# Optimization experiments

Hardware: AMD Instinct MI355X
Metric: run time of the kernel (lower is better)

The kernel has to match this reference:

```python
import jax, jax.numpy as jnp
import numpy as np

B, S, D, DFF = 4, 2048, 1024, 4096
EPS = 1e-5


def layernorm(x, gamma, beta):
    mu = jnp.mean(x, axis=-1, keepdims=True)
    var = jnp.var(x, axis=-1, keepdims=True)
    return (x - mu) * jax.lax.rsqrt(var + EPS) * gamma + beta


def attention(Q, K, V, causal):
    d_k = Q.shape[-1]
    scores = jnp.einsum('bqd,bkd->bqk', Q, K) / jnp.sqrt(jnp.asarray(d_k, Q.dtype))
    if causal:
        q_len, k_len = scores.shape[-2], scores.shape[-1]
        mask = jnp.tril(jnp.ones((q_len, k_len), dtype=bool))
        scores = jnp.where(mask[None], scores, jnp.asarray(-jnp.inf, scores.dtype))
    w = jax.nn.softmax(scores, axis=-1)
    return jnp.einsum('bqk,bkd->bqd', w, V)


def setup_inputs() -> dict:
    key = jax.random.key(0)
    ks = jax.random.split(key, 12)
    sd = 0.02
    return {
        'y': jax.random.normal(ks[0], (B, S, D), jnp.float32),
        'Z': jax.random.normal(ks[1], (B, S, D), jnp.float32),
        'w1': jax.random.normal(ks[2], (D, DFF), jnp.float32) * sd,
        'b1': jnp.zeros((DFF,), jnp.float32),
        'w2': jax.random.normal(ks[3], (DFF, D), jnp.float32) * sd,
        'b2': jnp.zeros((D,), jnp.float32),
        'g1': jnp.ones((D,), jnp.float32), 'beta1': jnp.zeros((D,), jnp.float32),
        'g2': jnp.ones((D,), jnp.float32), 'beta2': jnp.zeros((D,), jnp.float32),
        'g3': jnp.ones((D,), jnp.float32), 'beta3': jnp.zeros((D,), jnp.float32),
    }


def reference(y, Z, w1, b1, w2, b2, g1, beta1, g2, beta2, g3, beta3):
    # masked (causal) self-attention, single head over full d_model
    sa = attention(y, y, y, causal=True)
    y = layernorm(y + sa, g1, beta1)
    # cross-attention to encoder memory Z
    ca = attention(y, Z, Z, causal=False)
    y = layernorm(y + ca, g2, beta2)
    # position-wise FFN
    h = jax.nn.relu(jnp.einsum('bsd,df->bsf', y, w1) + b1)
    ff = jnp.einsum('bsf,fd->bsd', h, w2) + b2
    y = layernorm(y + ff, g3, beta3)
    return y
```

## Files before the change

### kernel.cpp

```cpp
#include <hip/hip_runtime.h>
#include <hip/hip_bf16.h>


#define Bb 4
#define Ss 2048
#define Dd 1024
#define Ff 4096

typedef __attribute__((ext_vector_type(4))) float f32x4;
typedef __attribute__((ext_vector_type(8))) short bf16x8;
typedef __attribute__((ext_vector_type(8))) unsigned short u16x8;
typedef __attribute__((ext_vector_type(4))) unsigned short u16x4;

__device__ __forceinline__ unsigned short f2bf(float f) {
  unsigned u = __float_as_uint(f);
  u += 0x7FFFu + ((u >> 16) & 1u);
  return (unsigned short)(u >> 16);
}
__device__ __forceinline__ float bf2f(unsigned short h) {
  return __uint_as_float(((unsigned)h) << 16);
}

__device__ __forceinline__ void gload_lds16(const void* g, void* l) {
  __builtin_amdgcn_global_load_lds((const __attribute__((address_space(1))) void*)g,
                                   (__attribute__((address_space(3))) void*)l, 16, 0, 0);
}

__device__ __forceinline__ int xcd8(int orig, int n) {
  int q = n >> 3, r = n & 7;
  int x = orig & 7;
  int base = x < r ? x * (q + 1) : r * (q + 1) + (x - r) * q;
  return base + (orig >> 3);
}

__global__ __launch_bounds__(256) void k_transpose_cast(const float* __restrict__ in,
                                                        unsigned short* __restrict__ outT,
                                                        unsigned short* __restrict__ outR,
                                                        int R, int C) {
  __shared__ float t[32][33];
  size_t bo = (size_t)blockIdx.z * R * C;
  const float* pin = in + bo;
  unsigned short* poutT = outT + bo;
  unsigned short* poutR = outR ? outR + bo : nullptr;
  int c0 = blockIdx.x * 32, r0 = blockIdx.y * 32;
  int tx = threadIdx.x, ty = threadIdx.y;
#pragma unroll
  for (int i = 0; i < 4; i++) {
    float v = pin[(size_t)(r0 + ty + i * 8) * C + c0 + tx];
    t[ty + i * 8][tx] = v;
    if (poutR) poutR[(size_t)(r0 + ty + i * 8) * C + c0 + tx] = f2bf(v);
  }
  __syncthreads();
#pragma unroll
  for (int i = 0; i < 4; i++)
    poutT[(size_t)(c0 + ty + i * 8) * R + r0 + tx] = f2bf(t[tx][ty + i * 8]);
}

#define BAR() __builtin_amdgcn_s_barrier()
#define PRIO1() __builtin_amdgcn_s_setprio(1)
#define PRIO0() __builtin_amdgcn_s_setprio(0)
#define LGKM0()                                          \
  {                                                      \
    asm volatile("s_waitcnt lgkmcnt(0)" ::: "memory");   \
    __builtin_amdgcn_sched_barrier(0);                   \
  }

#define LDA8(arr, mh, bo)                                                       \
  {                                                                             \
    _Pragma("unroll") for (int j_ = 0; j_ < QM; ++j_) {                         \
      _Pragma("unroll") for (int kh_ = 0; kh_ < 2; ++kh_) {                     \
        arr[j_][kh_] =                                                          \
            *(const bf16x8*)(lds + (bo) + ((mh)*QM + j_) * 2048 + aof[kh_]);    \
      }                                                                         \
    }                                                                           \
  }

#define LDB8(arr, nh, bo)                                                       \
  {                                                                             \
    _Pragma("unroll") for (int n_ = 0; n_ < 2; ++n_) {                          \
      _Pragma("unroll") for (int kh_ = 0; kh_ < 2; ++kh_) {                     \
        arr[n_][kh_] =                                                          \
            *(const bf16x8*)(lds + (bo) + ((nh)*2 + n_) * 2048 + bof[kh_]);     \
      }                                                                         \
    }                                                                           \
  }

#define MMQ(aarr, barr, mh, nh)                                                 \
  {                                                                             \
    _Pragma("unroll") for (int j_ = 0; j_ < QM; ++j_) {                         \
      _Pragma("unroll") for (int n_ = 0; n_ < 2; ++n_) {                        \
        _Pragma("unroll") for (int kh_ = 0; kh_ < 2; ++kh_) {                   \
          acc[(mh)*QM + j_][(nh)*2 + n_] = __builtin_amdgcn_mfma_f32_16x16x32_bf16( \
              aarr[j_][kh_], barr[n_][kh_], acc[(mh)*QM + j_][(nh)*2 + n_], 0, 0, 0); \
        }                                                                       \
      }                                                                         \
    }                                                                           \
  }

#define EPILOGUE(MR_, WMS_)                                                     \
  {                                                                             \
    const int colb = j0 + wc * 64 + fr;                                         \
    const int rowb = i0 + wr * (WMS_) + (kq << 2);                              \
    const size_t cb = (size_t)bz * bsC;                                         \
    _Pragma("unroll") for (int m = 0; m < (MR_); ++m) {                         \
      _Pragma("unroll") for (int r = 0; r < 4; ++r) {                           \
        size_t ro = cb + (size_t)(rowb + m * 16 + r) * ldc;                     \
        _Pragma("unroll") for (int n = 0; n < 4; ++n) {                         \
          float v = acc[m][n][r];                                               \
          int col = colb + n * 16;                                              \
          if (EPI == 0) Cb[ro + col] = f2bf(v * scale);                         \
          else if (EPI == 1) Cf[ro + col] = v;                                  \
          else if (EPI == 2) Cb[ro + col] = f2bf(fmaxf(v + bias[col], 0.f));    \
          else Cf[ro + col] = v + bias[col];                                    \
        }                                                                       \
      }                                                                         \
    }                                                                           \
  }

template <int EPI, bool CAUSAL>
__global__ __launch_bounds__(512) void k_gemm8(
    const unsigned short* __restrict__ Ag, const unsigned short* __restrict__ Bg,
    float* __restrict__ Cf, unsigned short* __restrict__ Cb,
    const float* __restrict__ bias, int K, int lda, int ldb, int ldc,
    long bsA, long bsB, long bsC, float scale) {
  constexpr int QM = 4;
  constexpr int ABYTES = 32768, BBYTES = 32768;
  __shared__ alignas(16) char lds[2 * ABYTES + 2 * BBYTES];

  int i0, j0;
  if (CAUSAL) {
    int t = xcd8(blockIdx.x, gridDim.x);
    int ti = (int)((sqrtf(8.f * t + 1.f) - 1.f) * 0.5f);
    while ((ti + 1) * (ti + 2) / 2 <= t) ++ti;
    while (ti * (ti + 1) / 2 > t) --ti;
    i0 = ti * 256;
    j0 = (t - ti * (ti + 1) / 2) * 256;
  } else {
    int lin = xcd8(blockIdx.y * gridDim.x + blockIdx.x, gridDim.x * gridDim.y);
    i0 = (lin / gridDim.x) * 256;
    j0 = (lin % gridDim.x) * 256;
  }
  int bz = blockIdx.z;
  Ag += (size_t)bz * bsA;
  Bg += (size_t)bz * bsB;

  const int nk = K / 64;
  const int niter = nk / 2;

  const int tid = threadIdx.x;
  const int w = tid >> 6, lane = tid & 63;
  const int wr = w >> 2, wc = w & 3;

  const int srow = (w << 3) + (lane >> 3);
  const int bcs = (lane & 7) ^ (lane >> 3);
  const unsigned short* As = Ag + (size_t)(i0 + srow) * lda + bcs * 8;
  const unsigned short* Bs = Bg + (size_t)(j0 + srow) * ldb + bcs * 8;
  char* ldsAw = lds + w * 1024;
  char* ldsBw = lds + 2 * ABYTES + w * 1024;

  auto stA = [&](int kt, int hf) {
    int ks = kt < nk ? kt : nk - 1;
#pragma unroll
    for (int l = 0; l < 2; ++l)
      gload_lds16(As + (size_t)(hf * 128 + l * 64) * lda + ks * 64,
                  ldsAw + (kt & 1) * ABYTES + hf * 128 * 128 + l * 8192);
  };
  auto stB = [&](int kt, int hf) {
    int ks = kt < nk ? kt : nk - 1;
#pragma unroll
    for (int l = 0; l < 2; ++l)
      gload_lds16(Bs + (size_t)(hf * 128 + l * 64) * ldb + ks * 64,
                  ldsBw + (kt & 1) * BBYTES + hf * 128 * 128 + l * 8192);
  };

  const int fr = lane & 15, kq = lane >> 4;
  const int rA = wr * 128 + fr;
  const int rB = wc * 64 + fr;
  unsigned aof[2], bof[2];
  aof[0] = rA * 128 + ((kq ^ (rA & 7)) << 4);
  aof[1] = rA * 128 + (((kq + 4) ^ (rA & 7)) << 4);
  bof[0] = 2 * ABYTES + rB * 128 + ((kq ^ (rB & 7)) << 4);
  bof[1] = 2 * ABYTES + rB * 128 + (((kq + 4) ^ (rB & 7)) << 4);
  constexpr int A0 = 0, A1 = ABYTES, B0 = 0, B1 = BBYTES;

  f32x4 acc[8][4];
#pragma unroll
  for (int m = 0; m < 8; ++m)
#pragma unroll
    for (int n = 0; n < 4; ++n) acc[m][n] = (f32x4){0.f, 0.f, 0.f, 0.f};

  bf16x8 a0[QM][2], a1[QM][2], b0[2][2], b1[2][2];

  stA(0, 0); stA(0, 1); stB(0, 0); stB(0, 1);
  stA(1, 0); stA(1, 1); stB(1, 0);
  asm volatile("s_waitcnt vmcnt(6)" ::: "memory");
  BAR();

  for (int t = 0; t < niter; ++t) {
    const int ka = 2 * t + 2, kb = 2 * t + 3;
    LDA8(a0, 0, A0); LDB8(b0, 0, B0);
    stB(2 * t + 1, 1);
    BAR(); LGKM0(); PRIO1(); MMQ(a0, b0, 0, 0); PRIO0(); BAR();
    LDA8(a1, 1, A0);
    BAR(); LGKM0(); PRIO1(); MMQ(a1, b0, 1, 0); PRIO0(); BAR();
    LDB8(b1, 1, B0);
    stA(ka, 0);
    BAR(); LGKM0(); PRIO1(); MMQ(a1, b1, 1, 1); PRIO0(); BAR();
    stA(ka, 1); stB(ka, 0);
    asm volatile("s_waitcnt vmcnt(6)" ::: "memory");
    BAR(); PRIO1(); MMQ(a0, b1, 0, 1); PRIO0(); BAR();
    LDA8(a0, 0, A1); LDB8(b0, 0, B1);
    stB(ka, 1);
    BAR(); LGKM0(); PRIO1(); MMQ(a0, b0, 0, 0); PRIO0(); BAR();
    LDA8(a1, 1, A1);
    BAR(); LGKM0(); PRIO1(); MMQ(a1, b0, 1, 0); PRIO0(); BAR();
    LDB8(b1, 1, B1);
    stA(kb, 0);
    BAR(); LGKM0(); PRIO1(); MMQ(a1, b1, 1, 1); PRIO0(); BAR();
    stA(kb, 1); stB(kb, 0);
    asm volatile("s_waitcnt vmcnt(6)" ::: "memory");
    BAR(); PRIO1(); MMQ(a0, b1, 0, 1); PRIO0(); BAR();
  }
  EPILOGUE(8, 128)
}

template <int EPI, bool KCAP>
__global__ __launch_bounds__(512) void k_gemm4(
    const unsigned short* __restrict__ Ag, const unsigned short* __restrict__ Bg,
    float* __restrict__ Cf, unsigned short* __restrict__ Cb,
    const float* __restrict__ bias, int K, int lda, int ldb, int ldc,
    long bsA, long bsB, long bsC, float scale) {
  constexpr int QM = 4;
  constexpr int ABYTES = 16384, BBYTES = 32768;
  __shared__ alignas(16) char lds[2 * ABYTES + 2 * BBYTES];

  int lin = xcd8(blockIdx.y * gridDim.x + blockIdx.x, gridDim.x * gridDim.y);
  int i0 = (lin / gridDim.x) * 128;
  int j0 = (lin % gridDim.x) * 256;
  int bz = blockIdx.z;
  Ag += (size_t)bz * bsA;
  Bg += (size_t)bz * bsB;

  int nk = K / 64;
  if (KCAP) {
    int cap = i0 / 64 + 2;
    nk = nk < cap ? nk : cap;
  }
  const int niter = nk / 2;

  const int tid = threadIdx.x;
  const int w = tid >> 6, lane = tid & 63;
  const int wr = w >> 2, wc = w & 3;

  const int srow = (w << 3) + (lane >> 3);
  const int bcs = (lane & 7) ^ (lane >> 3);
  const unsigned short* As = Ag + (size_t)(i0 + srow) * lda + bcs * 8;
  const unsigned short* Bs = Bg + (size_t)(j0 + srow) * ldb + bcs * 8;
  char* ldsAw = lds + w * 1024;
  char* ldsBw = lds + 2 * ABYTES + w * 1024;

  auto stA2 = [&](int kt) {
    int ks = kt < nk ? kt : nk - 1;
#pragma unroll
    for (int hf = 0; hf < 2; ++hf)
      gload_lds16(As + (size_t)(hf * 64) * lda + ks * 64,
                  ldsAw + (kt & 1) * ABYTES + hf * 64 * 128);
  };
  auto stB2 = [&](int kt) {
    int ks = kt < nk ? kt : nk - 1;
#pragma unroll
    for (int hf = 0; hf < 2; ++hf)
#pragma unroll
      for (int l = 0; l < 2; ++l)
        gload_lds16(Bs + (size_t)(hf * 128 + l * 64) * ldb + ks * 64,
                    ldsBw + (kt & 1) * BBYTES + hf * 128 * 128 + l * 8192);
  };

  const int fr = lane & 15, kq = lane >> 4;
  const int rA = wr * 64 + fr;
  const int rB = wc * 64 + fr;
  unsigned aof[2], bof[2];
  aof[0] = rA * 128 + ((kq ^ (rA & 7)) << 4);
  aof[1] = rA * 128 + (((kq + 4) ^ (rA & 7)) << 4);
  bof[0] = 2 * ABYTES + rB * 128 + ((kq ^ (rB & 7)) << 4);
  bof[1] = 2 * ABYTES + rB * 128 + (((kq + 4) ^ (rB & 7)) << 4);
  constexpr int A0 = 0, A1 = ABYTES, B0 = 0, B1 = BBYTES;

  f32x4 acc[4][4];
#pragma unroll
  for (int m = 0; m < 4; ++m)
#pragma unroll
    for (int n = 0; n < 4; ++n) acc[m][n] = (f32x4){0.f, 0.f, 0.f, 0.f};

  bf16x8 a[QM][2], b0[2][2], b1[2][2];

  stA2(0); stB2(0); stA2(1);
  asm volatile("s_waitcnt vmcnt(2)" ::: "memory");
  BAR();

  for (int t = 0; t < niter; ++t) {
    const int ka = 2 * t + 2, kb = 2 * t + 3;
    LDA8(a, 0, A0); LDB8(b0, 0, B0);
    stB2(2 * t + 1);
    BAR(); LGKM0(); PRIO1(); MMQ(a, b0, 0, 0); PRIO0(); BAR();
    LDB8(b1, 1, B0);
    stA2(ka);
    asm volatile("s_waitcnt vmcnt(2)" ::: "memory");
    BAR(); LGKM0(); PRIO1(); MMQ(a, b1, 0, 1); PRIO0(); BAR();
    LDA8(a, 0, A1); LDB8(b0, 0, B1);
    stB2(ka);
    BAR(); LGKM0(); PRIO1(); MMQ(a, b0, 0, 0); PRIO0(); BAR();
    LDB8(b1, 1, B1);
    stA2(kb);
    asm volatile("s_waitcnt vmcnt(2)" ::: "memory");
    BAR(); LGKM0(); PRIO1(); MMQ(a, b1, 0, 1); PRIO0(); BAR();
  }
  EPILOGUE(4, 64)
}

template <bool CAUSAL>
__global__ __launch_bounds__(256) void k_softmax(unsigned short* __restrict__ scores) {
  int row = blockIdx.x;
  int i = row & (Ss - 1);
  unsigned short* src = scores + (size_t)row * Ss;
  int nv = CAUSAL ? i + 1 : Ss;
  int t = threadIdx.x;
  int w = t >> 6, lane = t & 63;
  u16x8 raw = *(const u16x8*)(src + t * 8);
  float v[8];
  float mx = -1e30f;
#pragma unroll
  for (int k = 0; k < 8; k++) {
    int j = t * 8 + k;
    v[k] = (j < nv) ? bf2f(raw[k]) : -1e30f;
    mx = fmaxf(mx, v[k]);
  }
#pragma unroll
  for (int o = 32; o; o >>= 1) mx = fmaxf(mx, __shfl_xor(mx, o));
  __shared__ float red[8];
  if (lane == 0) red[w] = mx;
  __syncthreads();
  mx = fmaxf(fmaxf(red[0], red[1]), fmaxf(red[2], red[3]));
  float sum = 0.f;
#pragma unroll
  for (int k = 0; k < 8; k++) {
    int j = t * 8 + k;
    float e = (j < nv) ? __expf(v[k] - mx) : 0.f;
    v[k] = e;
    sum += e;
  }
#pragma unroll
  for (int o = 32; o; o >>= 1) sum += __shfl_xor(sum, o);
  if (lane == 0) red[4 + w] = sum;
  __syncthreads();
  sum = red[4] + red[5] + red[6] + red[7];
  float inv = 1.f / sum;
  u16x8 r;
#pragma unroll
  for (int k = 0; k < 8; k++) r[k] = f2bf(v[k] * inv);
  *(u16x8*)(src + t * 8) = r;
}

__global__ __launch_bounds__(256) void k_add_ln(const float* __restrict__ a,
                                                const float* __restrict__ b,
                                                const float* __restrict__ g,
                                                const float* __restrict__ be,
                                                float* __restrict__ outf,
                                                unsigned short* __restrict__ outb) {
  int row = blockIdx.x;
  size_t o = (size_t)row * Dd;
  int t = threadIdx.x;
  f32x4 xa = *(const f32x4*)(a + o + t * 4);
  f32x4 xb = *(const f32x4*)(b + o + t * 4);
  f32x4 x = xa + xb;
  float s = x[0] + x[1] + x[2] + x[3];
  float q = x[0] * x[0] + x[1] * x[1] + x[2] * x[2] + x[3] * x[3];
  int w = t >> 6, lane = t & 63;
#pragma unroll
  for (int of = 32; of; of >>= 1) {
    s += __shfl_xor(s, of);
    q += __shfl_xor(q, of);
  }
  __shared__ float red[8];
  if (lane == 0) {
    red[w] = s;
    red[4 + w] = q;
  }
  __syncthreads();
  s = red[0] + red[1] + red[2] + red[3];
  q = red[4] + red[5] + red[6] + red[7];
  float mean = s * (1.f / Dd);
  float var = q * (1.f / Dd) - mean * mean;
  float rstd = rsqrtf(var + 1e-5f);
  f32x4 gv = *(const f32x4*)(g + t * 4);
  f32x4 bv = *(const f32x4*)(be + t * 4);
  f32x4 y;
#pragma unroll
  for (int k = 0; k < 4; k++) y[k] = (x[k] - mean) * rstd * gv[k] + bv[k];
  *(f32x4*)(outf + o + t * 4) = y;
  if (outb) {
    u16x4 r;
    r[0] = f2bf(y[0]); r[1] = f2bf(y[1]); r[2] = f2bf(y[2]); r[3] = f2bf(y[3]);
    *(u16x4*)(outb + o + t * 4) = r;
  }
}

extern "C" void kernel_launch(void* const* d_in, const int* in_sizes, int n_in, void* d_out,
                              int out_size, void* d_ws, size_t ws_size, hipStream_t stream) {
  (void)in_sizes; (void)n_in; (void)out_size; (void)ws_size;
  const float* y   = (const float*)d_in[0];
  const float* Z   = (const float*)d_in[1];
  const float* w1  = (const float*)d_in[2];
  const float* b1  = (const float*)d_in[3];
  const float* w2  = (const float*)d_in[4];
  const float* b2  = (const float*)d_in[5];
  const float* g1  = (const float*)d_in[6];
  const float* be1 = (const float*)d_in[7];
  const float* g2  = (const float*)d_in[8];
  const float* be2 = (const float*)d_in[9];
  const float* g3  = (const float*)d_in[10];
  const float* be3 = (const float*)d_in[11];
  float* out = (float*)d_out;

  char* ws = (char*)d_ws;
  const size_t MB = 1024ull * 1024ull;
  unsigned short* T   = (unsigned short*)(ws);
  unsigned short* Zbf = (unsigned short*)(ws + 16 * MB);
  unsigned short* ybf = (unsigned short*)(ws + 32 * MB);
  unsigned short* w1t = (unsigned short*)(ws + 48 * MB);
  unsigned short* w2t = (unsigned short*)(ws + 56 * MB);
  unsigned short* sc  = (unsigned short*)(ws + 64 * MB);
  unsigned short* h   = (unsigned short*)(ws + 64 * MB);
  float* res          = (float*)(ws + 128 * MB);
  float* attn         = (float*)d_out;

  dim3 b256(256), b512(512);
  const float scl = 1.f / 32.f;

  k_transpose_cast<<<dim3(Dd / 32, Ss / 32, Bb), dim3(32, 8), 0, stream>>>(y, T, ybf, Ss, Dd);
  k_gemm8<0, true><<<dim3(36, 1, Bb), b512, 0, stream>>>(
      ybf, ybf, nullptr, sc, nullptr, Dd, Dd, Dd, Ss, (long)Ss * Dd, (long)Ss * Dd,
      (long)Ss * Ss, scl);
  k_softmax<true><<<dim3(Bb * Ss), b256, 0, stream>>>(sc);
  k_gemm4<1, true><<<dim3(Dd / 256, Ss / 128, Bb), b512, 0, stream>>>(
      sc, T, attn, nullptr, nullptr, Ss, Ss, Ss, Dd,
      (long)Ss * Ss, (long)Dd * Ss, (long)Ss * Dd, 1.f);
  k_add_ln<<<dim3(Bb * Ss), b256, 0, stream>>>(y, attn, g1, be1, res, ybf);

  k_transpose_cast<<<dim3(Dd / 32, Ss / 32, Bb), dim3(32, 8), 0, stream>>>(Z, T, Zbf, Ss, Dd);
  k_gemm8<0, false><<<dim3(Ss / 256, Ss / 256, Bb), b512, 0, stream>>>(
      ybf, Zbf, nullptr, sc, nullptr, Dd, Dd, Dd, Ss, (long)Ss * Dd, (long)Ss * Dd,
      (long)Ss * Ss, scl);
  k_softmax<false><<<dim3(Bb * Ss), b256, 0, stream>>>(sc);
  k_gemm4<1, false><<<dim3(Dd / 256, Ss / 128, Bb), b512, 0, stream>>>(
      sc, T, attn, nullptr, nullptr, Ss, Ss, Ss, Dd,
      (long)Ss * Ss, (long)Dd * Ss, (long)Ss * Dd, 1.f);
  k_add_ln<<<dim3(Bb * Ss), b256, 0, stream>>>(res, attn, g2, be2, res, ybf);

  k_transpose_cast<<<dim3(Ff / 32, Dd / 32, 1), dim3(32, 8), 0, stream>>>(w1, w1t, nullptr, Dd, Ff);
  k_transpose_cast<<<dim3(Dd / 32, Ff / 32, 1), dim3(32, 8), 0, stream>>>(w2, w2t, nullptr, Ff, Dd);
  k_gemm8<2, false><<<dim3(Ff / 256, (Bb * Ss) / 256, 1), b512, 0, stream>>>(
      ybf, w1t, nullptr, h, b1, Dd, Dd, Dd, Ff, 0L, 0L, 0L, 1.f);
  k_gemm4<3, false><<<dim3(Dd / 256, (Bb * Ss) / 128, 1), b512, 0, stream>>>(
      h, w2t, attn, nullptr, b2, Ff, Ff, Ff, Dd, 0L, 0L, 0L, 1.f);
  k_add_ln<<<dim3(Bb * Ss), b256, 0, stream>>>(res, attn, g3, be3, out, nullptr);
}
```

Measured before the change: 403.4 us.

## Fuse residual add into GEMM epilogue, reschedule gemm8 loads, skip masked softmax tiles

Moves the residual addition into the epilogue of the PV and FFN2 GEMMs, so the layernorm kernels read one fp32 tensor per row instead of two. The gemm8 main loop now issues B-fragment LDS reads one stage earlier and uses a tighter vmcnt wait, which aims to overlap LDS reads with MFMA work. In the causal softmax, threads entirely past the 128-aligned causal boundary skip their loads and stores. The cost is an extra residual read in the GEMM epilogues and a more delicate wait and barrier schedule in gemm8.

After: 396.7 us. No clear change (-1.7%).

```diff
diff --git a/kernel.cpp b/kernel.cpp
--- a/kernel.cpp
+++ b/kernel.cpp
@@ -109,9 +109,9 @@
           float v = acc[m][n][r];                                               \
           int col = colb + n * 16;                                              \
           if (EPI == 0) Cb[ro + col] = f2bf(v * scale);                         \
-          else if (EPI == 1) Cf[ro + col] = v;                                  \
           else if (EPI == 2) Cb[ro + col] = f2bf(fmaxf(v + bias[col], 0.f));    \
-          else Cf[ro + col] = v + bias[col];                                    \
+          else if (EPI == 4) Cf[ro + col] = v + resid[ro + col];                \
+          else Cf[ro + col] = v + bias[col] + resid[ro + col];                  \
         }                                                                       \
       }                                                                         \
     }                                                                           \
@@ -121,8 +121,8 @@
 __global__ __launch_bounds__(512) void k_gemm8(
     const unsigned short* __restrict__ Ag, const unsigned short* __restrict__ Bg,
     float* __restrict__ Cf, unsigned short* __restrict__ Cb,
-    const float* __restrict__ bias, int K, int lda, int ldb, int ldc,
-    long bsA, long bsB, long bsC, float scale) {
+    const float* __restrict__ bias, const float* __restrict__ resid,
+    int K, int lda, int ldb, int ldc, long bsA, long bsB, long bsC, float scale) {
   constexpr int QM = 4;
   constexpr int ABYTES = 32768, BBYTES = 32768;
   __shared__ alignas(16) char lds[2 * ABYTES + 2 * BBYTES];
@@ -195,31 +195,34 @@
   stA(1, 0); stA(1, 1); stB(1, 0);
   asm volatile("s_waitcnt vmcnt(6)" ::: "memory");
   BAR();
+  LDB8(b0, 0, B0);
 
   for (int t = 0; t < niter; ++t) {
     const int ka = 2 * t + 2, kb = 2 * t + 3;
-    LDA8(a0, 0, A0); LDB8(b0, 0, B0);
+    LDA8(a0, 0, A0);
     stB(2 * t + 1, 1);
     BAR(); LGKM0(); PRIO1(); MMQ(a0, b0, 0, 0); PRIO0(); BAR();
     LDA8(a1, 1, A0);
     BAR(); LGKM0(); PRIO1(); MMQ(a1, b0, 1, 0); PRIO0(); BAR();
     LDB8(b1, 1, B0);
     stA(ka, 0);
+    asm volatile("s_waitcnt vmcnt(2)" ::: "memory");
     BAR(); LGKM0(); PRIO1(); MMQ(a1, b1, 1, 1); PRIO0(); BAR();
+    LDB8(b0, 0, B1);
     stA(ka, 1); stB(ka, 0);
-    asm volatile("s_waitcnt vmcnt(6)" ::: "memory");
-    BAR(); PRIO1(); MMQ(a0, b1, 0, 1); PRIO0(); BAR();
-    LDA8(a0, 0, A1); LDB8(b0, 0, B1);
+    BAR(); LGKM0(); PRIO1(); MMQ(a0, b1, 0, 1); PRIO0(); BAR();
+    LDA8(a0, 0, A1);
     stB(ka, 1);
     BAR(); LGKM0(); PRIO1(); MMQ(a0, b0, 0, 0); PRIO0(); BAR();
     LDA8(a1, 1, A1);
     BAR(); LGKM0(); PRIO1(); MMQ(a1, b0, 1, 0); PRIO0(); BAR();
     LDB8(b1, 1, B1);
     stA(kb, 0);
+    asm volatile("s_waitcnt vmcnt(2)" ::: "memory");
     BAR(); LGKM0(); PRIO1(); MMQ(a1, b1, 1, 1); PRIO0(); BAR();
+    LDB8(b0, 0, B0);
     stA(kb, 1); stB(kb, 0);
-    asm volatile("s_waitcnt vmcnt(6)" ::: "memory");
-    BAR(); PRIO1(); MMQ(a0, b1, 0, 1); PRIO0(); BAR();
+    BAR(); LGKM0(); PRIO1(); MMQ(a0, b1, 0, 1); PRIO0(); BAR();
   }
   EPILOGUE(8, 128)
 }
@@ -228,8 +231,8 @@
 __global__ __launch_bounds__(512) void k_gemm4(
     const unsigned short* __restrict__ Ag, const unsigned short* __restrict__ Bg,
     float* __restrict__ Cf, unsigned short* __restrict__ Cb,
-    const float* __restrict__ bias, int K, int lda, int ldb, int ldc,
-    long bsA, long bsB, long bsC, float scale) {
+    const float* __restrict__ bias, const float* __restrict__ resid,
+    int K, int lda, int ldb, int ldc, long bsA, long bsB, long bsC, float scale) {
   constexpr int QM = 4;
   constexpr int ABYTES = 16384, BBYTES = 32768;
   __shared__ alignas(16) char lds[2 * ABYTES + 2 * BBYTES];
@@ -324,16 +327,23 @@
   int i = row & (Ss - 1);
   unsigned short* src = scores + (size_t)row * Ss;
   int nv = CAUSAL ? i + 1 : Ss;
+  int nb = CAUSAL ? ((i & ~127) + 128) : Ss;
   int t = threadIdx.x;
   int w = t >> 6, lane = t & 63;
-  u16x8 raw = *(const u16x8*)(src + t * 8);
+  bool act = t * 8 < nb;
   float v[8];
   float mx = -1e30f;
-#pragma unroll
-  for (int k = 0; k < 8; k++) {
-    int j = t * 8 + k;
-    v[k] = (j < nv) ? bf2f(raw[k]) : -1e30f;
-    mx = fmaxf(mx, v[k]);
+  if (act) {
+    u16x8 raw = *(const u16x8*)(src + t * 8);
+#pragma unroll
+    for (int k = 0; k < 8; k++) {
+      int j = t * 8 + k;
+      v[k] = (j < nv) ? bf2f(raw[k]) : -1e30f;
+      mx = fmaxf(mx, v[k]);
+    }
+  } else {
+#pragma unroll
+    for (int k = 0; k < 8; k++) v[k] = -1e30f;
   }
 #pragma unroll
   for (int o = 32; o; o >>= 1) mx = fmaxf(mx, __shfl_xor(mx, o));
@@ -344,8 +354,7 @@
   float sum = 0.f;
 #pragma unroll
   for (int k = 0; k < 8; k++) {
-    int j = t * 8 + k;
-    float e = (j < nv) ? __expf(v[k] - mx) : 0.f;
+    float e = (v[k] > -1e29f) ? __expf(v[k] - mx) : 0.f;
     v[k] = e;
     sum += e;
   }
@@ -355,24 +364,23 @@
   __syncthreads();
   sum = red[4] + red[5] + red[6] + red[7];
   float inv = 1.f / sum;
-  u16x8 r;
-#pragma unroll
-  for (int k = 0; k < 8; k++) r[k] = f2bf(v[k] * inv);
-  *(u16x8*)(src + t * 8) = r;
-}
-
-__global__ __launch_bounds__(256) void k_add_ln(const float* __restrict__ a,
-                                                const float* __restrict__ b,
-                                                const float* __restrict__ g,
-                                                const float* __restrict__ be,
-                                                float* __restrict__ outf,
-                                                unsigned short* __restrict__ outb) {
+  if (act) {
+    u16x8 r;
+#pragma unroll
+    for (int k = 0; k < 8; k++) r[k] = f2bf(v[k] * inv);
+    *(u16x8*)(src + t * 8) = r;
+  }
+}
+
+__global__ __launch_bounds__(256) void k_ln(const float* __restrict__ a,
+                                            const float* __restrict__ g,
+                                            const float* __restrict__ be,
+                                            float* __restrict__ outf,
+                                            unsigned short* __restrict__ outb) {
   int row = blockIdx.x;
   size_t o = (size_t)row * Dd;
   int t = threadIdx.x;
-  f32x4 xa = *(const f32x4*)(a + o + t * 4);
-  f32x4 xb = *(const f32x4*)(b + o + t * 4);
-  f32x4 x = xa + xb;
+  f32x4 x = *(const f32x4*)(a + o + t * 4);
   float s = x[0] + x[1] + x[2] + x[3];
   float q = x[0] * x[0] + x[1] * x[1] + x[2] * x[2] + x[3] * x[3];
   int w = t >> 6, lane = t & 63;
@@ -439,29 +447,29 @@
 
   k_transpose_cast<<<dim3(Dd / 32, Ss / 32, Bb), dim3(32, 8), 0, stream>>>(y, T, ybf, Ss, Dd);
   k_gemm8<0, true><<<dim3(36, 1, Bb), b512, 0, stream>>>(
-      ybf, ybf, nullptr, sc, nullptr, Dd, Dd, Dd, Ss, (long)Ss * Dd, (long)Ss * Dd,
-      (long)Ss * Ss, scl);
+      ybf, ybf, nullptr, sc, nullptr, nullptr, Dd, Dd, Dd, Ss,
+      (long)Ss * Dd, (long)Ss * Dd, (long)Ss * Ss, scl);
   k_softmax<true><<<dim3(Bb * Ss), b256, 0, stream>>>(sc);
-  k_gemm4<1, true><<<dim3(Dd / 256, Ss / 128, Bb), b512, 0, stream>>>(
-      sc, T, attn, nullptr, nullptr, Ss, Ss, Ss, Dd,
+  k_gemm4<4, true><<<dim3(Dd / 256, Ss / 128, Bb), b512, 0, stream>>>(
+      sc, T, attn, nullptr, nullptr, y, Ss, Ss, Ss, Dd,
       (long)Ss * Ss, (long)Dd * Ss, (long)Ss * Dd, 1.f);
-  k_add_ln<<<dim3(Bb * Ss), b256, 0, stream>>>(y, attn, g1, be1, res, ybf);
+  k_ln<<<dim3(Bb * Ss), b256, 0, stream>>>(attn, g1, be1, res, ybf);
 
   k_transpose_cast<<<dim3(Dd / 32, Ss / 32, Bb), dim3(32, 8), 0, stream>>>(Z, T, Zbf, Ss, Dd);
   k_gemm8<0, false><<<dim3(Ss / 256, Ss / 256, Bb), b512, 0, stream>>>(
-      ybf, Zbf, nullptr, sc, nullptr, Dd, Dd, Dd, Ss, (long)Ss * Dd, (long)Ss * Dd,
-      (long)Ss * Ss, scl);
+      ybf, Zbf, nullptr, sc, nullptr, nullptr, Dd, Dd, Dd, Ss,
+      (long)Ss * Dd, (long)Ss * Dd, (long)Ss * Ss, scl);
   k_softmax<false><<<dim3(Bb * Ss), b256, 0, stream>>>(sc);
-  k_gemm4<1, false><<<dim3(Dd / 256, Ss / 128, Bb), b512, 0, stream>>>(
-      sc, T, attn, nullptr, nullptr, Ss, Ss, Ss, Dd,
+  k_gemm4<4, false><<<dim3(Dd / 256, Ss / 128, Bb), b512, 0, stream>>>(
+      sc, T, attn, nullptr, nullptr, res, Ss, Ss, Ss, Dd,
       (long)Ss * Ss, (long)Dd * Ss, (long)Ss * Dd, 1.f);
-  k_add_ln<<<dim3(Bb * Ss), b256, 0, stream>>>(res, attn, g2, be2, res, ybf);
+  k_ln<<<dim3(Bb * Ss), b256, 0, stream>>>(attn, g2, be2, res, ybf);
 
   k_transpose_cast<<<dim3(Ff / 32, Dd / 32, 1), dim3(32, 8), 0, stream>>>(w1, w1t, nullptr, Dd, Ff);
   k_transpose_cast<<<dim3(Dd / 32, Ff / 32, 1), dim3(32, 8), 0, stream>>>(w2, w2t, nullptr, Ff, Dd);
   k_gemm8<2, false><<<dim3(Ff / 256, (Bb * Ss) / 256, 1), b512, 0, stream>>>(
-      ybf, w1t, nullptr, h, b1, Dd, Dd, Dd, Ff, 0L, 0L, 0L, 1.f);
-  k_gemm4<3, false><<<dim3(Dd / 256, (Bb * Ss) / 128, 1), b512, 0, stream>>>(
-      h, w2t, attn, nullptr, b2, Ff, Ff, Ff, Dd, 0L, 0L, 0L, 1.f);
-  k_add_ln<<<dim3(Bb * Ss), b256, 0, stream>>>(res, attn, g3, be3, out, nullptr);
-}
+      ybf, w1t, nullptr, h, b1, nullptr, Dd, Dd, Dd, Ff, 0L, 0L, 0L, 1.f);
+  k_gemm4<5, false><<<dim3(Dd / 256, (Bb * Ss) / 128, 1), b512, 0, stream>>>(
+      h, w2t, attn, nullptr, b2, res, Ff, Ff, Ff, Dd, 0L, 0L, 0L, 1.f);
+  k_ln<<<dim3(Bb * Ss), b256, 0, stream>>>(attn, g3, be3, out, nullptr);
+}
```
